# Kernel optimization log

Hardware: AMD Instinct MI355X
Metric: run time of the kernel (lower is better)

The kernel has to match this reference:

```python
import jax, jax.numpy as jnp
import numpy as np

HID = 512
HEADS = 8
D = HID // HEADS          # att_size = 64
B = 64                    # number of graphs
L = 1024                  # bonds per graph (equal-length scopes)
SCALE = D ** (-0.5)
EPS = 1e-5


def setup_inputs() -> dict:
    key = jax.random.key(0)
    ks = jax.random.split(key, 9)
    f = lambda k, s, sc=1.0: jax.random.normal(k, s, dtype=jnp.float32) * sc
    edge_attr = f(ks[0], (B * L, HID))
    # contiguous equal-length scopes: (start, length) per graph
    scopes = np.stack([np.arange(B, dtype=np.int64) * L,
                       np.full(B, L, dtype=np.int64)], axis=1)
    return {
        "edge_attr": edge_attr,
        "batch_scopes": jnp.asarray(scopes),
        "Wq": f(ks[1], (HID, HID), 0.03),   # torch Linear weight [out, in]
        "Wk": f(ks[2], (HID, HID), 0.03),
        "Wv": f(ks[3], (HID, HID), 0.03),
        "Wr": f(ks[4], (D, D), 0.1),
        "w_alpha": f(ks[5], (D,)),
        "w_beta": f(ks[6], (D,)),
        "Wo": f(ks[7], (HID, HID), 0.03),
        "bo": jnp.zeros((HID,), jnp.float32),
        "ln_g": jnp.ones((HID,), jnp.float32),
        "ln_b": jnp.zeros((HID,), jnp.float32),
    }


def reference(edge_attr, batch_scopes, Wq, Wk, Wv, Wr, w_alpha, w_beta,
              Wo, bo, ln_g, ln_b):
    # Scopes are contiguous, equal length L -> pad_sequence == reshape
    padded = edge_attr.reshape(B, L, HID)

    def proj(W):  # (B, L, HID) @ W.T -> (B, heads, L, D)
        return jnp.einsum('blh,dh->bld', padded, W).reshape(B, L, HEADS, D).transpose(0, 2, 1, 3)

    b_q = proj(Wq)
    b_k = proj(Wk)
    b_v = proj(Wv)

    # softmax over the head-feature dim (faithful to dim=-1 in torch code)
    alpha = jax.nn.softmax(b_q * w_alpha * SCALE, axis=-1)
    global_q = jnp.sum(alpha * b_q, axis=2)            # (B, heads, D), sum over L

    p = global_q[:, :, None, :] * b_k                  # (B, heads, L, D)
    beta = jax.nn.softmax(p * w_beta * SCALE, axis=-1)
    global_k = jnp.sum(beta * p, axis=2)               # (B, heads, D)

    kv = global_k[:, :, None, :] * b_v                 # (B, heads, L, D)
    kv_out = jnp.einsum('bhld,ed->bhle', kv, Wr)
    att = jax.nn.relu(kv_out + b_q)                    # dropout p=0 (eval)

    att = att.transpose(0, 2, 1, 3).reshape(B, L, HID)
    out = jnp.einsum('blh,oh->blo', att, Wo) + bo

    # LayerNorm over last dim
    mu = jnp.mean(out, axis=-1, keepdims=True)
    var = jnp.mean((out - mu) ** 2, axis=-1, keepdims=True)
    out = (out - mu) * jax.lax.rsqrt(var + EPS) * ln_g + ln_b

    # unpad + concat == flatten for equal-length contiguous scopes
    return out.reshape(B * L, HID)
```

## Files before the change

kernel.cpp:

```cpp
#include <hip/hip_runtime.h>
#include <stdint.h>


#define SCALE_F 0.125f
#define EPSF 1e-5f

typedef __attribute__((ext_vector_type(8))) short short8;
typedef __attribute__((ext_vector_type(4))) float float4v;
typedef unsigned short ushort_t;

__device__ __forceinline__ ushort_t f2bf(float f) {
  uint32_t u = __builtin_bit_cast(uint32_t, f);
  u += 0x7fffu + ((u >> 16) & 1u);
  return (ushort_t)(u >> 16);
}
__device__ __forceinline__ float bf2f(ushort_t s) {
  uint32_t u = ((uint32_t)s) << 16;
  return __builtin_bit_cast(float, u);
}

__device__ __forceinline__ void gload16(const void* g, void* l) {
  __builtin_amdgcn_global_load_lds(
      (__attribute__((address_space(1))) char*)(char*)const_cast<void*>(g),
      (__attribute__((address_space(3))) char*)(char*)l, 16, 0, 0);
}

__global__ __launch_bounds__(256) void cvt_x(const float* __restrict__ X,
                                             ushort_t* __restrict__ Xb) {
  const int i = blockIdx.x * 256 + threadIdx.x;
  const float4v* src = (const float4v*)X;
  float4v v0 = src[(size_t)i * 2];
  float4v v1 = src[(size_t)i * 2 + 1];
  short8 o;
#pragma unroll
  for (int j = 0; j < 4; ++j) {
    o[j]     = (short)f2bf(v0[j]);
    o[j + 4] = (short)f2bf(v1[j]);
  }
  ((short8*)Xb)[i] = o;
}

__global__ __launch_bounds__(256) void cvt_w(const float* __restrict__ Wq,
                                             const float* __restrict__ Wk,
                                             const float* __restrict__ Wv,
                                             const float* __restrict__ Wo,
                                             ushort_t* __restrict__ Wqkv,
                                             ushort_t* __restrict__ Wob) {
  const int i = blockIdx.x * 256 + threadIdx.x;
  if (i < 262144)        Wqkv[i] = f2bf(Wq[i]);
  else if (i < 524288)   Wqkv[i] = f2bf(Wk[i - 262144]);
  else if (i < 786432)   Wqkv[i] = f2bf(Wv[i - 524288]);
  else                   Wob[i - 786432] = f2bf(Wo[i - 786432]);
}

template <int MODE>
__global__ __launch_bounds__(256) void gemm_bt(const ushort_t* __restrict__ A,
                                               const ushort_t* __restrict__ Bm,
                                               void* __restrict__ Cout,
                                               const float* __restrict__ bias,
                                               int N, int K) {
  __shared__ __align__(16) ushort_t As[128 * 64];
  __shared__ __align__(16) ushort_t Bs[128 * 64];
  const int tn = blockIdx.x, tm = blockIdx.y;
  const int row0 = tm * 128, col0 = tn * 128;
  const int tid = threadIdx.x, wid = tid >> 6, lane = tid & 63;
  const int wr = wid >> 1, wc = wid & 1;
  const int lr = lane & 15, lk = lane >> 4;
  float4v acc[4][4] = {};
  const int KB = K * 2;
  for (int kt = 0; kt < K; kt += 64) {
    __syncthreads();
#pragma unroll
    for (int i = 0; i < 4; ++i) {
      const int dst = i * 4096 + wid * 1024;
      const int off = dst + lane * 16;
      const int r = off >> 7, cb = off & 127;
      gload16((const char*)A + (size_t)(row0 + r) * KB + kt * 2 + cb, (char*)As + dst);
      gload16((const char*)Bm + (size_t)(col0 + r) * KB + kt * 2 + cb, (char*)Bs + dst);
    }
    asm volatile("s_waitcnt vmcnt(0)" ::: "memory");
    __syncthreads();
#pragma unroll
    for (int ks = 0; ks < 2; ++ks) {
      short8 a[4], b[4];
#pragma unroll
      for (int mi = 0; mi < 4; ++mi)
        a[mi] = *(const short8*)((const char*)As + (wr * 64 + mi * 16 + lr) * 128 + ks * 64 + lk * 16);
#pragma unroll
      for (int ni = 0; ni < 4; ++ni)
        b[ni] = *(const short8*)((const char*)Bs + (wc * 64 + ni * 16 + lr) * 128 + ks * 64 + lk * 16);
#pragma unroll
      for (int mi = 0; mi < 4; ++mi)
#pragma unroll
        for (int ni = 0; ni < 4; ++ni)
          acc[mi][ni] = __builtin_amdgcn_mfma_f32_16x16x32_bf16(a[mi], b[ni], acc[mi][ni], 0, 0, 0);
    }
  }
#pragma unroll
  for (int mi = 0; mi < 4; ++mi)
#pragma unroll
    for (int ni = 0; ni < 4; ++ni) {
      const int col = col0 + wc * 64 + ni * 16 + lr;
#pragma unroll
      for (int r = 0; r < 4; ++r) {
        const int row = row0 + wr * 64 + mi * 16 + lk * 4 + r;
        const float v = acc[mi][ni][r];
        if (MODE == 0)
          ((ushort_t*)Cout)[(size_t)row * N + col] = f2bf(v);
        else
          ((float*)Cout)[(size_t)row * N + col] = v + bias[col];
      }
    }
}

__global__ __launch_bounds__(512) void reduce_att(const ushort_t* __restrict__ QKV,
                                                  const float* __restrict__ Wr,
                                                  const float* __restrict__ w_alpha,
                                                  const float* __restrict__ w_beta,
                                                  ushort_t* __restrict__ att) {
  const int bh = blockIdx.x, b = bh >> 3, h = bh & 7;
  const int tid = threadIdx.x, wid = tid >> 6, lane = tid & 63;
  const int rsub = lane >> 3, dch = lane & 7;
  __shared__ float red[8][64];
  __shared__ float gq_s[64];
  __shared__ float gk_s[64];
  __shared__ __align__(16) ushort_t Ml[64 * 72];
  float wa[8], wb[8];
#pragma unroll
  for (int j = 0; j < 8; ++j) {
    wa[j] = w_alpha[dch * 8 + j] * SCALE_F;
    wb[j] = w_beta[dch * 8 + j] * SCALE_F;
  }
  const size_t base = (size_t)b * 1024;
  float acc[8] = {0, 0, 0, 0, 0, 0, 0, 0};
  for (int it = 0; it < 16; ++it) {
    const size_t t = base + it * 64 + wid * 8 + rsub;
    short8 raw = *(const short8*)(QKV + t * 1536 + h * 64 + dch * 8);
    float q[8], s[8];
#pragma unroll
    for (int j = 0; j < 8; ++j) { q[j] = bf2f((ushort_t)raw[j]); s[j] = q[j] * wa[j]; }
    float m = s[0];
#pragma unroll
    for (int j = 1; j < 8; ++j) m = fmaxf(m, s[j]);
    m = fmaxf(m, __shfl_xor(m, 1)); m = fmaxf(m, __shfl_xor(m, 2)); m = fmaxf(m, __shfl_xor(m, 4));
    float e[8], sum = 0.f;
#pragma unroll
    for (int j = 0; j < 8; ++j) { e[j] = __expf(s[j] - m); sum += e[j]; }
    sum += __shfl_xor(sum, 1); sum += __shfl_xor(sum, 2); sum += __shfl_xor(sum, 4);
    const float inv = 1.0f / sum;
#pragma unroll
    for (int j = 0; j < 8; ++j) acc[j] += e[j] * inv * q[j];
  }
#pragma unroll
  for (int msk = 8; msk < 64; msk <<= 1)
#pragma unroll
    for (int j = 0; j < 8; ++j) acc[j] += __shfl_xor(acc[j], msk);
  if (lane < 8) {
#pragma unroll
    for (int j = 0; j < 8; ++j) red[wid][lane * 8 + j] = acc[j];
  }
  __syncthreads();
  if (tid < 64) {
    float s = 0.f;
#pragma unroll
    for (int w = 0; w < 8; ++w) s += red[w][tid];
    gq_s[tid] = s;
  }
  __syncthreads();
  float gq[8];
#pragma unroll
  for (int j = 0; j < 8; ++j) gq[j] = gq_s[dch * 8 + j];
  float gkacc[8] = {0, 0, 0, 0, 0, 0, 0, 0};
  for (int it = 0; it < 16; ++it) {
    const size_t t = base + it * 64 + wid * 8 + rsub;
    short8 raw = *(const short8*)(QKV + t * 1536 + 512 + h * 64 + dch * 8);
    float p[8], s[8];
#pragma unroll
    for (int j = 0; j < 8; ++j) { p[j] = gq[j] * bf2f((ushort_t)raw[j]); s[j] = p[j] * wb[j]; }
    float m = s[0];
#pragma unroll
    for (int j = 1; j < 8; ++j) m = fmaxf(m, s[j]);
    m = fmaxf(m, __shfl_xor(m, 1)); m = fmaxf(m, __shfl_xor(m, 2)); m = fmaxf(m, __shfl_xor(m, 4));
    float e[8], sum = 0.f;
#pragma unroll
    for (int j = 0; j < 8; ++j) { e[j] = __expf(s[j] - m); sum += e[j]; }
    sum += __shfl_xor(sum, 1); sum += __shfl_xor(sum, 2); sum += __shfl_xor(sum, 4);
    const float inv = 1.0f / sum;
#pragma unroll
    for (int j = 0; j < 8; ++j) gkacc[j] += e[j] * inv * p[j];
  }
#pragma unroll
  for (int msk = 8; msk < 64; msk <<= 1)
#pragma unroll
    for (int j = 0; j < 8; ++j) gkacc[j] += __shfl_xor(gkacc[j], msk);
  if (lane < 8) {
#pragma unroll
    for (int j = 0; j < 8; ++j) red[wid][lane * 8 + j] = gkacc[j];
  }
  __syncthreads();
  if (tid < 64) {
    float s = 0.f;
#pragma unroll
    for (int w = 0; w < 8; ++w) s += red[w][tid];
    gk_s[tid] = s;
  }
  __syncthreads();
  for (int i = tid; i < 4096; i += 512) {
    const int e = i >> 6, d = i & 63;
    Ml[e * 72 + d] = f2bf(Wr[i] * gk_s[d]);
  }
  __syncthreads();
  const int lr = lane & 15, lk = lane >> 4;
  short8 bfr[4][2];
#pragma unroll
  for (int ni = 0; ni < 4; ++ni)
#pragma unroll
    for (int ks = 0; ks < 2; ++ks)
      bfr[ni][ks] = *(const short8*)&Ml[(ni * 16 + lr) * 72 + ks * 32 + lk * 8];
  const size_t tw = base + wid * 128;
  for (int c = 0; c < 2; ++c) {
    float4v oacc[4][4] = {};
#pragma unroll
    for (int ks = 0; ks < 2; ++ks) {
      short8 a[4];
#pragma unroll
      for (int mi = 0; mi < 4; ++mi) {
        const size_t t = tw + c * 64 + mi * 16 + lr;
        a[mi] = *(const short8*)(QKV + t * 1536 + 1024 + h * 64 + ks * 32 + lk * 8);
      }
#pragma unroll
      for (int mi = 0; mi < 4; ++mi)
#pragma unroll
        for (int ni = 0; ni < 4; ++ni)
          oacc[mi][ni] = __builtin_amdgcn_mfma_f32_16x16x32_bf16(a[mi], bfr[ni][ks], oacc[mi][ni], 0, 0, 0);
    }
#pragma unroll
    for (int mi = 0; mi < 4; ++mi)
#pragma unroll
      for (int ni = 0; ni < 4; ++ni)
#pragma unroll
        for (int r = 0; r < 4; ++r) {
          const size_t t = tw + c * 64 + mi * 16 + lk * 4 + r;
          const int e = ni * 16 + lr;
          float v = oacc[mi][ni][r] + bf2f(QKV[t * 1536 + h * 64 + e]);
          v = fmaxf(v, 0.0f);
          att[t * 512 + h * 64 + e] = f2bf(v);
        }
  }
}

__global__ __launch_bounds__(512, 2) void gemm_ln(const ushort_t* __restrict__ A,
                                                  const ushort_t* __restrict__ Bm,
                                                  float* __restrict__ out,
                                                  const float* __restrict__ bo,
                                                  const float* __restrict__ lng,
                                                  const float* __restrict__ lnb) {
  __shared__ __align__(16) ushort_t As[2][128 * 32];
  __shared__ __align__(16) ushort_t Bs[2][512 * 32];
  __shared__ float red_s[4][128][2];
  __shared__ float tot_s[128][2];
  const int tid = threadIdx.x, wid = tid >> 6, lane = tid & 63;
  const int wr = wid >> 2, wc = wid & 3;
  const int lr = lane & 15, lk = lane >> 4;
  const int row0 = blockIdx.x * 128;
  float4v acc[4][8] = {};

  const int la = lane * 16;
  const int ar = wid * 16 + (lane >> 2);
  const int acb = (lane & 3) * 16;

  auto stage = [&](int buf, int s) {
    const int k0b = s * 64;
    gload16((const char*)A + (size_t)(row0 + ar) * 1024 + k0b + acb,
            (char*)&As[buf][0] + wid * 1024);
#pragma unroll
    for (int i = 0; i < 4; ++i) {
      const int dst = (wid * 4 + i) * 1024;
      const int br = (dst + la) >> 6;
      const int bcb = la & 63;
      gload16((const char*)Bm + (size_t)br * 1024 + k0b + bcb,
              (char*)&Bs[buf][0] + dst);
    }
  };

  stage(0, 0);
  __syncthreads();
  for (int s = 0; s < 16; ++s) {
    const int buf = s & 1;
    if (s < 15) stage(buf ^ 1, s + 1);
    short8 af[4], bf[8];
#pragma unroll
    for (int mi = 0; mi < 4; ++mi)
      af[mi] = *(const short8*)((const char*)&As[buf][0] + (wr * 64 + mi * 16 + lr) * 64 + lk * 16);
#pragma unroll
    for (int ni = 0; ni < 8; ++ni)
      bf[ni] = *(const short8*)((const char*)&Bs[buf][0] + (wc * 128 + ni * 16 + lr) * 64 + lk * 16);
#pragma unroll
    for (int mi = 0; mi < 4; ++mi)
#pragma unroll
      for (int ni = 0; ni < 8; ++ni)
        acc[mi][ni] = __builtin_amdgcn_mfma_f32_16x16x32_bf16(af[mi], bf[ni], acc[mi][ni], 0, 0, 0);
    __syncthreads();
  }

  float bov[8], gv[8], bv[8];
#pragma unroll
  for (int ni = 0; ni < 8; ++ni) {
    const int c = wc * 128 + ni * 16 + lr;
    bov[ni] = bo[c]; gv[ni] = lng[c]; bv[ni] = lnb[c];
  }
#pragma unroll
  for (int mi = 0; mi < 4; ++mi)
#pragma unroll
    for (int ni = 0; ni < 8; ++ni)
#pragma unroll
      for (int r = 0; r < 4; ++r)
        acc[mi][ni][r] += bov[ni];
#pragma unroll
  for (int mi = 0; mi < 4; ++mi)
#pragma unroll
    for (int r = 0; r < 4; ++r) {
      float s = 0.f, q = 0.f;
#pragma unroll
      for (int ni = 0; ni < 8; ++ni) { const float v = acc[mi][ni][r]; s += v; q += v * v; }
      s += __shfl_xor(s, 1); q += __shfl_xor(q, 1);
      s += __shfl_xor(s, 2); q += __shfl_xor(q, 2);
      s += __shfl_xor(s, 4); q += __shfl_xor(q, 4);
      s += __shfl_xor(s, 8); q += __shfl_xor(q, 8);
      if (lr == 0) {
        const int rb = wr * 64 + mi * 16 + lk * 4 + r;
        red_s[wc][rb][0] = s;
        red_s[wc][rb][1] = q;
      }
    }
  __syncthreads();
  if (tid < 128) {
    tot_s[tid][0] = red_s[0][tid][0] + red_s[1][tid][0] + red_s[2][tid][0] + red_s[3][tid][0];
    tot_s[tid][1] = red_s[0][tid][1] + red_s[1][tid][1] + red_s[2][tid][1] + red_s[3][tid][1];
  }
  __syncthreads();
#pragma unroll
  for (int mi = 0; mi < 4; ++mi)
#pragma unroll
    for (int r = 0; r < 4; ++r) {
      const int rb = wr * 64 + mi * 16 + lk * 4 + r;
      const float mu = tot_s[rb][0] * (1.f / 512.f);
      const float var = tot_s[rb][1] * (1.f / 512.f) - mu * mu;
      const float rs = rsqrtf(var + EPSF);
      float* op = out + (size_t)(row0 + rb) * 512 + wc * 128 + lr;
#pragma unroll
      for (int ni = 0; ni < 8; ++ni)
        op[ni * 16] = (acc[mi][ni][r] - mu) * rs * gv[ni] + bv[ni];
    }
}

extern "C" void kernel_launch(void* const* d_in, const int* in_sizes, int n_in,
                              void* d_out, int out_size, void* d_ws, size_t ws_size,
                              hipStream_t stream) {
  const float* X       = (const float*)d_in[0];
  const float* Wq      = (const float*)d_in[2];
  const float* Wk      = (const float*)d_in[3];
  const float* Wv      = (const float*)d_in[4];
  const float* Wr      = (const float*)d_in[5];
  const float* w_alpha = (const float*)d_in[6];
  const float* w_beta  = (const float*)d_in[7];
  const float* Wo      = (const float*)d_in[8];
  const float* bo      = (const float*)d_in[9];
  const float* ln_g    = (const float*)d_in[10];
  const float* ln_b    = (const float*)d_in[11];

  char* ws = (char*)d_ws;
  ushort_t* Xb   = (ushort_t*)(ws);
  ushort_t* Wqkv = (ushort_t*)(ws + 67108864);
  ushort_t* Wob  = (ushort_t*)(ws + 68681728);
  ushort_t* QKV  = (ushort_t*)(ws + 69206016);
  ushort_t* att  = Xb;
  float* out = (float*)d_out;

  hipLaunchKernelGGL(cvt_x, dim3(16384), dim3(256), 0, stream, X, Xb);
  hipLaunchKernelGGL(cvt_w, dim3(4096), dim3(256), 0, stream, Wq, Wk, Wv, Wo, Wqkv, Wob);
  hipLaunchKernelGGL((gemm_bt<0>), dim3(12, 512), dim3(256), 0, stream,
                     Xb, Wqkv, (void*)QKV, (const float*)nullptr, 1536, 512);
  hipLaunchKernelGGL(reduce_att, dim3(512), dim3(512), 0, stream,
                     QKV, Wr, w_alpha, w_beta, att);
  hipLaunchKernelGGL(gemm_ln, dim3(512), dim3(512), 0, stream,
                     att, Wob, out, bo, ln_g, ln_b);
}
```

Before: 403.2 us.

## Replace QKV GEMM with 256x256 pipelined, swizzled, prioritized MFMA kernel

```diff
diff --git a/kernel.cpp b/kernel.cpp
--- a/kernel.cpp
+++ b/kernel.cpp
@@ -24,6 +24,10 @@
       (__attribute__((address_space(1))) char*)(char*)const_cast<void*>(g),
       (__attribute__((address_space(3))) char*)(char*)l, 16, 0, 0);
 }
+
+#define BARR() asm volatile("s_barrier" ::: "memory")
+#define LGKM0() do { asm volatile("s_waitcnt lgkmcnt(0)" ::: "memory"); \
+                     __builtin_amdgcn_sched_barrier(0); } while (0)
 
 __global__ __launch_bounds__(256) void cvt_x(const float* __restrict__ X,
                                              ushort_t* __restrict__ Xb) {
@@ -53,62 +57,147 @@
   else                   Wob[i - 786432] = f2bf(Wo[i - 786432]);
 }
 
-template <int MODE>
-__global__ __launch_bounds__(256) void gemm_bt(const ushort_t* __restrict__ A,
-                                               const ushort_t* __restrict__ Bm,
-                                               void* __restrict__ Cout,
-                                               const float* __restrict__ bias,
-                                               int N, int K) {
-  __shared__ __align__(16) ushort_t As[128 * 64];
-  __shared__ __align__(16) ushort_t Bs[128 * 64];
-  const int tn = blockIdx.x, tm = blockIdx.y;
-  const int row0 = tm * 128, col0 = tn * 128;
+__global__ __launch_bounds__(512, 2) void gemm8p(const ushort_t* __restrict__ A,
+                                                 const ushort_t* __restrict__ Bm,
+                                                 ushort_t* __restrict__ C) {
+  __shared__ __align__(16) char ldsA[65536];
+  __shared__ __align__(16) char ldsB[65536];
+  const int swz = (blockIdx.x & 7) * 192 + (blockIdx.x >> 3);
+  const int tm = swz / 6, tn = swz % 6;
+  const int row0 = tm * 256, col0 = tn * 256;
   const int tid = threadIdx.x, wid = tid >> 6, lane = tid & 63;
-  const int wr = wid >> 1, wc = wid & 1;
+  const int wr = wid >> 2, wc = wid & 3;
   const int lr = lane & 15, lk = lane >> 4;
-  float4v acc[4][4] = {};
-  const int KB = K * 2;
-  for (int kt = 0; kt < K; kt += 64) {
-    __syncthreads();
-#pragma unroll
-    for (int i = 0; i < 4; ++i) {
-      const int dst = i * 4096 + wid * 1024;
-      const int off = dst + lane * 16;
-      const int r = off >> 7, cb = off & 127;
-      gload16((const char*)A + (size_t)(row0 + r) * KB + kt * 2 + cb, (char*)As + dst);
-      gload16((const char*)Bm + (size_t)(col0 + r) * KB + kt * 2 + cb, (char*)Bs + dst);
-    }
-    asm volatile("s_waitcnt vmcnt(0)" ::: "memory");
-    __syncthreads();
-#pragma unroll
-    for (int ks = 0; ks < 2; ++ks) {
-      short8 a[4], b[4];
+  const int xr = (lr & 7) << 4;
+
+  auto stageA = [&](int kt, int h) {
+    const int slot = (2 * kt + h) & 3;
+    const int rowbase = row0 + h * 128;
+#pragma unroll
+    for (int i = 0; i < 2; ++i) {
+      const int o = i * 8192 + wid * 1024 + lane * 16;
+      const int r = o >> 7, x = o & 127;
+      gload16((const char*)A + (size_t)(rowbase + r) * 1024 + kt * 128 + (x ^ ((r & 7) << 4)),
+              ldsA + slot * 16384 + i * 8192 + wid * 1024);
+    }
+  };
+  auto stageB = [&](int kt, int h) {
+    const int slot = (2 * kt + h) & 3;
+    const int rowbase = col0 + h * 128;
+#pragma unroll
+    for (int i = 0; i < 2; ++i) {
+      const int o = i * 8192 + wid * 1024 + lane * 16;
+      const int r = o >> 7, x = o & 127;
+      gload16((const char*)Bm + (size_t)(rowbase + r) * 1024 + kt * 128 + (x ^ ((r & 7) << 4)),
+              ldsB + slot * 16384 + i * 8192 + wid * 1024);
+    }
+  };
+  auto rdA = [&](int t, int mi, int kk) -> short8 {
+    const int slot = (2 * t + wr) & 3;
+    return *(const short8*)(ldsA + slot * 16384 + (mi * 16 + lr) * 128 +
+                            ((kk * 64 + lk * 16) ^ xr));
+  };
+  auto rdB = [&](int t, int ni, int kk) -> short8 {
+    const int slot = (2 * t + (wc >> 1)) & 3;
+    return *(const short8*)(ldsB + slot * 16384 + ((wc & 1) * 64 + ni * 16 + lr) * 128 +
+                            ((kk * 64 + lk * 16) ^ xr));
+  };
+
+  float4v acc[8][4] = {};
+
+  stageA(0, 0); stageA(0, 1); stageB(0, 0); stageB(0, 1);
+  stageA(1, 0); stageA(1, 1); stageB(1, 0);
+  asm volatile("s_waitcnt vmcnt(6)" ::: "memory");
+  BARR();
+
+#pragma unroll
+  for (int t = 0; t < 8; ++t) {
+    short8 a0[4][2], a1[4][2], b0[2][2], b1[2][2];
+#pragma unroll
+    for (int mi = 0; mi < 4; ++mi)
+#pragma unroll
+      for (int kk = 0; kk < 2; ++kk) a0[mi][kk] = rdA(t, mi, kk);
+#pragma unroll
+    for (int ni = 0; ni < 2; ++ni)
+#pragma unroll
+      for (int kk = 0; kk < 2; ++kk) b0[ni][kk] = rdB(t, ni, kk);
+    if (t + 1 < 8) stageB(t + 1, 1);
+    BARR();
+    LGKM0();
+    __builtin_amdgcn_s_setprio(1);
+#pragma unroll
+    for (int kk = 0; kk < 2; ++kk)
 #pragma unroll
       for (int mi = 0; mi < 4; ++mi)
-        a[mi] = *(const short8*)((const char*)As + (wr * 64 + mi * 16 + lr) * 128 + ks * 64 + lk * 16);
-#pragma unroll
-      for (int ni = 0; ni < 4; ++ni)
-        b[ni] = *(const short8*)((const char*)Bs + (wc * 64 + ni * 16 + lr) * 128 + ks * 64 + lk * 16);
+#pragma unroll
+        for (int ni = 0; ni < 2; ++ni)
+          acc[mi][ni] = __builtin_amdgcn_mfma_f32_16x16x32_bf16(a0[mi][kk], b0[ni][kk], acc[mi][ni], 0, 0, 0);
+    __builtin_amdgcn_s_setprio(0);
+    __builtin_amdgcn_sched_barrier(0);
+    BARR();
+#pragma unroll
+    for (int mi = 0; mi < 4; ++mi)
+#pragma unroll
+      for (int kk = 0; kk < 2; ++kk) a1[mi][kk] = rdA(t, mi + 4, kk);
+#pragma unroll
+    for (int ni = 0; ni < 2; ++ni)
+#pragma unroll
+      for (int kk = 0; kk < 2; ++kk) b1[ni][kk] = rdB(t, ni + 2, kk);
+    BARR();
+    LGKM0();
+    __builtin_amdgcn_s_setprio(1);
+#pragma unroll
+    for (int kk = 0; kk < 2; ++kk)
 #pragma unroll
       for (int mi = 0; mi < 4; ++mi)
 #pragma unroll
-        for (int ni = 0; ni < 4; ++ni)
-          acc[mi][ni] = __builtin_amdgcn_mfma_f32_16x16x32_bf16(a[mi], b[ni], acc[mi][ni], 0, 0, 0);
-    }
-  }
-#pragma unroll
-  for (int mi = 0; mi < 4; ++mi)
+        for (int ni = 0; ni < 2; ++ni)
+          acc[mi][ni + 2] = __builtin_amdgcn_mfma_f32_16x16x32_bf16(a0[mi][kk], b1[ni][kk], acc[mi][ni + 2], 0, 0, 0);
+    __builtin_amdgcn_s_setprio(0);
+    __builtin_amdgcn_sched_barrier(0);
+    BARR();
+    if (t + 2 < 8) { stageA(t + 2, 0); stageA(t + 2, 1); }
+    __builtin_amdgcn_sched_barrier(0);
+    __builtin_amdgcn_s_setprio(1);
+#pragma unroll
+    for (int kk = 0; kk < 2; ++kk)
+#pragma unroll
+      for (int mi = 0; mi < 4; ++mi)
+#pragma unroll
+        for (int ni = 0; ni < 2; ++ni)
+          acc[mi + 4][ni] = __builtin_amdgcn_mfma_f32_16x16x32_bf16(a1[mi][kk], b0[ni][kk], acc[mi + 4][ni], 0, 0, 0);
+    __builtin_amdgcn_s_setprio(0);
+    __builtin_amdgcn_sched_barrier(0);
+    BARR();
+    if (t + 2 < 8) stageB(t + 2, 0);
+    __builtin_amdgcn_sched_barrier(0);
+    __builtin_amdgcn_s_setprio(1);
+#pragma unroll
+    for (int kk = 0; kk < 2; ++kk)
+#pragma unroll
+      for (int mi = 0; mi < 4; ++mi)
+#pragma unroll
+        for (int ni = 0; ni < 2; ++ni)
+          acc[mi + 4][ni + 2] = __builtin_amdgcn_mfma_f32_16x16x32_bf16(a1[mi][kk], b1[ni][kk], acc[mi + 4][ni + 2], 0, 0, 0);
+    __builtin_amdgcn_s_setprio(0);
+    __builtin_amdgcn_sched_barrier(0);
+    if (t < 6) {
+      asm volatile("s_waitcnt vmcnt(6)" ::: "memory");
+    } else if (t == 6) {
+      asm volatile("s_waitcnt vmcnt(0)" ::: "memory");
+    }
+    BARR();
+  }
+
+#pragma unroll
+  for (int mi = 0; mi < 8; ++mi)
 #pragma unroll
     for (int ni = 0; ni < 4; ++ni) {
       const int col = col0 + wc * 64 + ni * 16 + lr;
 #pragma unroll
       for (int r = 0; r < 4; ++r) {
-        const int row = row0 + wr * 64 + mi * 16 + lk * 4 + r;
-        const float v = acc[mi][ni][r];
-        if (MODE == 0)
-          ((ushort_t*)Cout)[(size_t)row * N + col] = f2bf(v);
-        else
-          ((float*)Cout)[(size_t)row * N + col] = v + bias[col];
+        const int row = row0 + wr * 128 + mi * 16 + lk * 4 + r;
+        C[(size_t)row * 1536 + col] = f2bf(acc[mi][ni][r]);
       }
     }
 }
@@ -379,8 +468,7 @@
 
   hipLaunchKernelGGL(cvt_x, dim3(16384), dim3(256), 0, stream, X, Xb);
   hipLaunchKernelGGL(cvt_w, dim3(4096), dim3(256), 0, stream, Wq, Wk, Wv, Wo, Wqkv, Wob);
-  hipLaunchKernelGGL((gemm_bt<0>), dim3(12, 512), dim3(256), 0, stream,
-                     Xb, Wqkv, (void*)QKV, (const float*)nullptr, 1536, 512);
+  hipLaunchKernelGGL(gemm8p, dim3(1536), dim3(512), 0, stream, Xb, Wqkv, QKV);
   hipLaunchKernelGGL(reduce_att, dim3(512), dim3(512), 0, stream,
                      QKV, Wr, w_alpha, w_beta, att);
   hipLaunchKernelGGL(gemm_ln, dim3(512), dim3(512), 0, stream,
```

Result: faster. 371.1 us (-8.0%).
